# Kernel tuning notes

Hardware: AMD Instinct MI355X
Metric: run time of the kernel (lower is better)

The kernel has to match this reference:

```python
import jax, jax.numpy as jnp
import numpy as np

B, S, D, DV = 64, 2048, 128, 256

def setup_inputs() -> dict:
    key = jax.random.key(0)
    ks = jax.random.split(key, 8)
    queries = jax.random.normal(ks[0], (B, S, D), dtype=jnp.float32)
    keys = jax.random.normal(ks[1], (B, S, D), dtype=jnp.float32)
    values = jax.random.normal(ks[2], (B, S, DV), dtype=jnp.float32)
    valid_lens = jax.random.randint(ks[3], (B,), 1, S + 1)
    # parameters (torch Linear stores weight as [out, in]; we keep math y = x @ W.T)
    w_v = jax.random.normal(ks[4], (2 * D,), dtype=jnp.float32) / np.sqrt(2 * D)   # Linear(256,1,bias=False)
    w2 = jax.random.normal(ks[5], (D, D), dtype=jnp.float32) / np.sqrt(D)          # Linear(128,128,bias=False)
    w_v2_w = jax.random.normal(ks[6], (D,), dtype=jnp.float32) / np.sqrt(D)        # Linear(128,1) weight
    w_v2_b = jax.random.normal(ks[7], (1,), dtype=jnp.float32) / np.sqrt(D)        # Linear(128,1) bias
    return {"queries": queries, "keys": keys, "values": values, "valid_lens": valid_lens,
            "w_v": w_v, "w2": w2, "w_v2_w": w_v2_w, "w_v2_b": w_v2_b}

def reference(queries, keys, values, valid_lens, w_v, w2, w_v2_w, w_v2_b):
    # path 1: concat + tanh + linear score -> [B,S]
    feats = jnp.tanh(jnp.concatenate((queries, keys), axis=-1))      # [B,S,256]
    scores1 = jnp.einsum("bsd,d->bs", feats, w_v)                    # squeeze(2)
    # path 2: linear + tanh + linear(+bias) + softmax over last dim of size 1 (=> all ones, kept faithful)
    feats2 = jnp.tanh(jnp.einsum("bsd,ed->bse", queries, w2))        # [B,S,128]
    s2 = jnp.einsum("bsd,d->bs", feats2, w_v2_w)[..., None] + w_v2_b  # [B,S,1]
    scores2 = jax.nn.softmax(s2, axis=-1)[..., 0]                    # [B,S]
    # blend (detached in original) + softmax over S
    blend = 0.5 * jax.lax.stop_gradient(scores1) + 0.5 * jax.lax.stop_gradient(scores2)
    scores = jax.nn.softmax(blend, axis=-1)[:, None, :]              # [B,1,S]
    # masked softmax with per-batch valid lengths
    mask = jnp.arange(S) < valid_lens[:, None]                       # [B,S]
    attn = jax.nn.softmax(jnp.where(mask[:, None, :], scores, -1e6), axis=-1)  # [B,1,S]
    # dropout is identity in eval mode
    return jnp.einsum("bqs,bsv->bqv", attn, values)                  # [B,1,DV]
```

## Files before the change

### kernel.cpp

```cpp
#include <hip/hip_runtime.h>

#define BB 64
#define SS 2048
#define DD 128
#define DDV 256
#define NCH 32
#define RPC 64

__device__ __forceinline__ float fast_tanh(float x) {
    const float t = __expf(2.0f * x);
    return 1.0f - 2.0f / (t + 1.0f);
}

__global__ __launch_bounds__(256) void k_blend(const float* __restrict__ q,
                                               const float* __restrict__ k,
                                               const float* __restrict__ wv,
                                               float* __restrict__ blend) {
    const int wave = threadIdx.x >> 6;
    const int lane = threadIdx.x & 63;
    const float* src = (lane < 32) ? q : k;
    const float4 w4  = *(const float4*)(wv + lane * 4);
    const int row0 = blockIdx.x * 16 + wave * 4;
#pragma unroll
    for (int i = 0; i < 4; ++i) {
        const int row  = row0 + i;
        const float4 x = *(const float4*)(src + (size_t)row * DD + (lane & 31) * 4);
        float acc = fast_tanh(x.x) * w4.x + fast_tanh(x.y) * w4.y
                  + fast_tanh(x.z) * w4.z + fast_tanh(x.w) * w4.w;
#pragma unroll
        for (int o = 32; o; o >>= 1) acc += __shfl_xor(acc, o, 64);
        if (lane == 0) blend[row] = 0.5f * acc + 0.5f;
    }
}

__global__ __launch_bounds__(1024) void k_weights(float* __restrict__ blend,
                                                  const int* __restrict__ valid) {
    __shared__ float r0[16], r1[16], r2[16], r3[16];
    const int b = blockIdx.x;
    const int t = threadIdx.x;
    const int wid = t >> 6, lane = t & 63;
    float* rowp = blend + (size_t)b * SS;

    const float v0 = rowp[t];
    const float v1 = rowp[t + 1024];

    float m = fmaxf(v0, v1);
#pragma unroll
    for (int o = 32; o; o >>= 1) m = fmaxf(m, __shfl_xor(m, o, 64));
    if (lane == 0) r0[wid] = m;
    __syncthreads();
    float m1 = r0[0];
#pragma unroll
    for (int i = 1; i < 16; i++) m1 = fmaxf(m1, r0[i]);

    const float e0 = expf(v0 - m1), e1 = expf(v1 - m1);
    float s = e0 + e1;
#pragma unroll
    for (int o = 32; o; o >>= 1) s += __shfl_xor(s, o, 64);
    if (lane == 0) r1[wid] = s;
    __syncthreads();
    float Z1 = 0.f;
#pragma unroll
    for (int i = 0; i < 16; i++) Z1 += r1[i];
    const float invZ1 = 1.f / Z1;
    const float p0 = e0 * invZ1, p1 = e1 * invZ1;

    const int L = valid[b];

    float mm = -1e30f;
    if (t < L)        mm = p0;
    if (t + 1024 < L) mm = fmaxf(mm, p1);
#pragma unroll
    for (int o = 32; o; o >>= 1) mm = fmaxf(mm, __shfl_xor(mm, o, 64));
    if (lane == 0) r2[wid] = mm;
    __syncthreads();
    float m2 = r2[0];
#pragma unroll
    for (int i = 1; i < 16; i++) m2 = fmaxf(m2, r2[i]);

    const float f0 = (t < L)        ? expf(p0 - m2) : 0.f;
    const float f1 = (t + 1024 < L) ? expf(p1 - m2) : 0.f;
    float s2 = f0 + f1;
#pragma unroll
    for (int o = 32; o; o >>= 1) s2 += __shfl_xor(s2, o, 64);
    if (lane == 0) r3[wid] = s2;
    __syncthreads();
    float Z2 = 0.f;
#pragma unroll
    for (int i = 0; i < 16; i++) Z2 += r3[i];
    const float invZ2 = 1.f / Z2;

    rowp[t]        = f0 * invZ2;
    rowp[t + 1024] = f1 * invZ2;
}

__global__ __launch_bounds__(256) void k_pv(const float* __restrict__ w,
                                            const float* __restrict__ values,
                                            const int* __restrict__ valid,
                                            float* __restrict__ partial) {
    const int c = blockIdx.x, b = blockIdx.y;
    const int t = threadIdx.x;
    const int wid = t >> 6, lane = t & 63;
    const int s0 = c * RPC;
    __shared__ float wsm[RPC];
    __shared__ float4 sacc[256];

    const int L = valid[b];
    float4 acc = {0.f, 0.f, 0.f, 0.f};
    if (s0 < L) {
        if (t < RPC) wsm[t] = w[(size_t)b * SS + s0 + t];
        __syncthreads();
        float wr[16];
        bool any = false;
#pragma unroll
        for (int i = 0; i < 16; i++) { wr[i] = wsm[wid * 16 + i]; any |= (wr[i] != 0.f); }
        if (any) {
            const float* vb = values + ((size_t)b * SS + s0 + wid * 16) * DDV + lane * 4;
#pragma unroll
            for (int i = 0; i < 16; i++) {
                const float4 v4 = *(const float4*)(vb + (size_t)i * DDV);
                acc.x += wr[i] * v4.x;
                acc.y += wr[i] * v4.y;
                acc.z += wr[i] * v4.z;
                acc.w += wr[i] * v4.w;
            }
        }
    }
    sacc[t] = acc;
    __syncthreads();
    if (t < 64) {
        const float4 a0 = sacc[t], a1 = sacc[t + 64], a2 = sacc[t + 128], a3 = sacc[t + 192];
        float4 r;
        r.x = a0.x + a1.x + a2.x + a3.x;
        r.y = a0.y + a1.y + a2.y + a3.y;
        r.z = a0.z + a1.z + a2.z + a3.z;
        r.w = a0.w + a1.w + a2.w + a3.w;
        *(float4*)(partial + ((size_t)(b * NCH + c)) * 256 + t * 4) = r;
    }
}

__global__ __launch_bounds__(256) void k_reduce(const float* __restrict__ partial,
                                                float* __restrict__ out) {
    const int b = blockIdx.x, t = threadIdx.x;
    float acc = 0.f;
#pragma unroll
    for (int c = 0; c < NCH; c++) acc += partial[((size_t)b * NCH + c) * 256 + t];
    out[(size_t)b * 256 + t] = acc;
}

extern "C" void kernel_launch(void* const* d_in, const int* in_sizes, int n_in,
                              void* d_out, int out_size, void* d_ws, size_t ws_size,
                              hipStream_t stream) {
    const float* q    = (const float*)d_in[0];
    const float* k    = (const float*)d_in[1];
    const float* v    = (const float*)d_in[2];
    const int*   vlen = (const int*)d_in[3];
    const float* wv   = (const float*)d_in[4];

    float* blend   = (float*)d_ws;
    float* partial = blend + (size_t)BB * SS;
    float* out     = (float*)d_out;

    k_blend <<<dim3(BB * SS / 16), dim3(256),  0, stream>>>(q, k, wv, blend);
    k_weights<<<dim3(BB),          dim3(1024), 0, stream>>>(blend, vlen);
    k_pv     <<<dim3(NCH, BB),     dim3(256),  0, stream>>>(blend, v, vlen, partial);
    k_reduce <<<dim3(BB),          dim3(256),  0, stream>>>(partial, out);
}
```

Measured before the change: 46.53 us.

## Compute softmax stats only and recompute weights inside PV kernel

The weights kernel now writes only per-batch softmax statistics (max, inverse sum for both softmaxes) instead of rewriting the full weight row, and the PV kernel recomputes each weight from the blend score and the stats. This removes a full write of the weight buffer. The blend kernel also drops the constant 0.5 offset (it cancels in the softmax), folds the 0.5 scale into the weights, handles 8 rows per wave instead of 4, and uses a hardware reciprocal in tanh. The cost is two extra exps per weight in the PV kernel.

New measurement: 45.22 us. 2.8% less time.

```diff
diff --git a/kernel.cpp b/kernel.cpp
--- a/kernel.cpp
+++ b/kernel.cpp
@@ -9,7 +9,7 @@
 
 __device__ __forceinline__ float fast_tanh(float x) {
     const float t = __expf(2.0f * x);
-    return 1.0f - 2.0f / (t + 1.0f);
+    return 1.0f - 2.0f * __builtin_amdgcn_rcpf(t + 1.0f);
 }
 
 __global__ __launch_bounds__(256) void k_blend(const float* __restrict__ q,
@@ -19,27 +19,29 @@
     const int wave = threadIdx.x >> 6;
     const int lane = threadIdx.x & 63;
     const float* src = (lane < 32) ? q : k;
-    const float4 w4  = *(const float4*)(wv + lane * 4);
-    const int row0 = blockIdx.x * 16 + wave * 4;
+    float4 w4 = *(const float4*)(wv + lane * 4);
+    w4.x *= 0.5f; w4.y *= 0.5f; w4.z *= 0.5f; w4.w *= 0.5f;
+    const int row0 = blockIdx.x * 32 + wave * 8;
+    const float* base = src + (size_t)row0 * DD + (lane & 31) * 4;
 #pragma unroll
-    for (int i = 0; i < 4; ++i) {
-        const int row  = row0 + i;
-        const float4 x = *(const float4*)(src + (size_t)row * DD + (lane & 31) * 4);
+    for (int i = 0; i < 8; ++i) {
+        const float4 x = *(const float4*)(base + (size_t)i * DD);
         float acc = fast_tanh(x.x) * w4.x + fast_tanh(x.y) * w4.y
                   + fast_tanh(x.z) * w4.z + fast_tanh(x.w) * w4.w;
 #pragma unroll
         for (int o = 32; o; o >>= 1) acc += __shfl_xor(acc, o, 64);
-        if (lane == 0) blend[row] = 0.5f * acc + 0.5f;
+        if (lane == 0) blend[row0 + i] = acc;
     }
 }
 
-__global__ __launch_bounds__(1024) void k_weights(float* __restrict__ blend,
-                                                  const int* __restrict__ valid) {
+__global__ __launch_bounds__(1024) void k_stats(const float* __restrict__ blend,
+                                                const int* __restrict__ valid,
+                                                float4* __restrict__ stats) {
     __shared__ float r0[16], r1[16], r2[16], r3[16];
     const int b = blockIdx.x;
     const int t = threadIdx.x;
     const int wid = t >> 6, lane = t & 63;
-    float* rowp = blend + (size_t)b * SS;
+    const float* rowp = blend + (size_t)b * SS;
 
     const float v0 = rowp[t];
     const float v1 = rowp[t + 1024];
@@ -63,13 +65,12 @@
 #pragma unroll
     for (int i = 0; i < 16; i++) Z1 += r1[i];
     const float invZ1 = 1.f / Z1;
-    const float p0 = e0 * invZ1, p1 = e1 * invZ1;
 
     const int L = valid[b];
 
     float mm = -1e30f;
-    if (t < L)        mm = p0;
-    if (t + 1024 < L) mm = fmaxf(mm, p1);
+    if (t < L)        mm = e0 * invZ1;
+    if (t + 1024 < L) mm = fmaxf(mm, e1 * invZ1);
 #pragma unroll
     for (int o = 32; o; o >>= 1) mm = fmaxf(mm, __shfl_xor(mm, o, 64));
     if (lane == 0) r2[wid] = mm;
@@ -78,9 +79,9 @@
 #pragma unroll
     for (int i = 1; i < 16; i++) m2 = fmaxf(m2, r2[i]);
 
-    const float f0 = (t < L)        ? expf(p0 - m2) : 0.f;
-    const float f1 = (t + 1024 < L) ? expf(p1 - m2) : 0.f;
-    float s2 = f0 + f1;
+    float s2 = 0.f;
+    if (t < L)        s2  = expf(e0 * invZ1 - m2);
+    if (t + 1024 < L) s2 += expf(e1 * invZ1 - m2);
 #pragma unroll
     for (int o = 32; o; o >>= 1) s2 += __shfl_xor(s2, o, 64);
     if (lane == 0) r3[wid] = s2;
@@ -88,13 +89,11 @@
     float Z2 = 0.f;
 #pragma unroll
     for (int i = 0; i < 16; i++) Z2 += r3[i];
-    const float invZ2 = 1.f / Z2;
-
-    rowp[t]        = f0 * invZ2;
-    rowp[t + 1024] = f1 * invZ2;
+    if (t == 0) stats[b] = make_float4(m1, invZ1, m2, 1.f / Z2);
 }
 
-__global__ __launch_bounds__(256) void k_pv(const float* __restrict__ w,
+__global__ __launch_bounds__(256) void k_pv(const float* __restrict__ blend,
+                                            const float4* __restrict__ stats,
                                             const float* __restrict__ values,
                                             const int* __restrict__ valid,
                                             float* __restrict__ partial) {
@@ -108,7 +107,14 @@
     const int L = valid[b];
     float4 acc = {0.f, 0.f, 0.f, 0.f};
     if (s0 < L) {
-        if (t < RPC) wsm[t] = w[(size_t)b * SS + s0 + t];
+        const float4 st = stats[b];
+        if (t < RPC) {
+            const int s = s0 + t;
+            float w = 0.f;
+            if (s < L)
+                w = expf(expf(blend[(size_t)b * SS + s] - st.x) * st.y - st.z) * st.w;
+            wsm[t] = w;
+        }
         __syncthreads();
         float wr[16];
         bool any = false;
@@ -157,12 +163,13 @@
     const int*   vlen = (const int*)d_in[3];
     const float* wv   = (const float*)d_in[4];
 
-    float* blend   = (float*)d_ws;
-    float* partial = blend + (size_t)BB * SS;
-    float* out     = (float*)d_out;
+    float*  blend   = (float*)d_ws;
+    float4* stats   = (float4*)(blend + (size_t)BB * SS);
+    float*  partial = (float*)(stats + BB);
+    float*  out     = (float*)d_out;
 
-    k_blend <<<dim3(BB * SS / 16), dim3(256),  0, stream>>>(q, k, wv, blend);
-    k_weights<<<dim3(BB),          dim3(1024), 0, stream>>>(blend, vlen);
-    k_pv     <<<dim3(NCH, BB),     dim3(256),  0, stream>>>(blend, v, vlen, partial);
-    k_reduce <<<dim3(BB),          dim3(256),  0, stream>>>(partial, out);
+    k_blend <<<dim3(BB * SS / 32), dim3(256),  0, stream>>>(q, k, wv, blend);
+    k_stats <<<dim3(BB),           dim3(1024), 0, stream>>>(blend, vlen, stats);
+    k_pv    <<<dim3(NCH, BB),      dim3(256),  0, stream>>>(blend, stats, v, vlen, partial);
+    k_reduce<<<dim3(BB),           dim3(256),  0, stream>>>(partial, out);
 }
```

## Fuse masked softmax and value reduction into one per-batch kernel

Applied to the files above, without the earlier changes.

Merges the weights, partial-PV and reduce kernels into a single kernel with one 1024-thread block per batch. It keeps the softmax weights in LDS and streams the value rows directly to the output, removing the partial buffer and two launches. The blend kernel now handles 32 rows per block, folds the 0.5 scale into the weights, drops the constant offset (safe because softmax is shift-invariant), and uses a hardware reciprocal inside tanh. The trade-off is that the value streaming, the dominant memory traffic, now runs on only 64 blocks, which may leave much of the GPU's bandwidth unused.

Result: slower. 51.40 us (+10.5%).

```diff
diff --git a/kernel.cpp b/kernel.cpp
--- a/kernel.cpp
+++ b/kernel.cpp
@@ -4,12 +4,10 @@
 #define SS 2048
 #define DD 128
 #define DDV 256
-#define NCH 32
-#define RPC 64
 
 __device__ __forceinline__ float fast_tanh(float x) {
     const float t = __expf(2.0f * x);
-    return 1.0f - 2.0f / (t + 1.0f);
+    return 1.0f - 2.0f * __builtin_amdgcn_rcpf(t + 1.0f);
 }
 
 __global__ __launch_bounds__(256) void k_blend(const float* __restrict__ q,
@@ -19,27 +17,32 @@
     const int wave = threadIdx.x >> 6;
     const int lane = threadIdx.x & 63;
     const float* src = (lane < 32) ? q : k;
-    const float4 w4  = *(const float4*)(wv + lane * 4);
-    const int row0 = blockIdx.x * 16 + wave * 4;
+    float4 w4 = *(const float4*)(wv + lane * 4);
+    w4.x *= 0.5f; w4.y *= 0.5f; w4.z *= 0.5f; w4.w *= 0.5f;
+    const int row0 = blockIdx.x * 32 + wave * 8;
+    const float* base = src + (size_t)row0 * DD + (lane & 31) * 4;
 #pragma unroll
-    for (int i = 0; i < 4; ++i) {
-        const int row  = row0 + i;
-        const float4 x = *(const float4*)(src + (size_t)row * DD + (lane & 31) * 4);
+    for (int i = 0; i < 8; ++i) {
+        const float4 x = *(const float4*)(base + (size_t)i * DD);
         float acc = fast_tanh(x.x) * w4.x + fast_tanh(x.y) * w4.y
                   + fast_tanh(x.z) * w4.z + fast_tanh(x.w) * w4.w;
 #pragma unroll
         for (int o = 32; o; o >>= 1) acc += __shfl_xor(acc, o, 64);
-        if (lane == 0) blend[row] = 0.5f * acc + 0.5f;
+        if (lane == 0) blend[row0 + i] = acc;
     }
 }
 
-__global__ __launch_bounds__(1024) void k_weights(float* __restrict__ blend,
-                                                  const int* __restrict__ valid) {
-    __shared__ float r0[16], r1[16], r2[16], r3[16];
+__global__ __launch_bounds__(1024) void k_batch(const float* __restrict__ blend,
+                                                const int* __restrict__ valid,
+                                                const float* __restrict__ values,
+                                                float* __restrict__ out) {
+    __shared__ float  wlds[SS];
+    __shared__ float4 sacc[16][64];
+    __shared__ float  r0[16], r1[16], r2[16], r3[16];
     const int b = blockIdx.x;
     const int t = threadIdx.x;
-    const int wid = t >> 6, lane = t & 63;
-    float* rowp = blend + (size_t)b * SS;
+    const int w = t >> 6, lane = t & 63;
+    const float* rowp = blend + (size_t)b * SS;
 
     const float v0 = rowp[t];
     const float v1 = rowp[t + 1024];
@@ -47,21 +50,21 @@
     float m = fmaxf(v0, v1);
 #pragma unroll
     for (int o = 32; o; o >>= 1) m = fmaxf(m, __shfl_xor(m, o, 64));
-    if (lane == 0) r0[wid] = m;
+    if (lane == 0) r0[w] = m;
     __syncthreads();
     float m1 = r0[0];
 #pragma unroll
-    for (int i = 1; i < 16; i++) m1 = fmaxf(m1, r0[i]);
+    for (int i = 1; i < 16; ++i) m1 = fmaxf(m1, r0[i]);
 
     const float e0 = expf(v0 - m1), e1 = expf(v1 - m1);
     float s = e0 + e1;
 #pragma unroll
     for (int o = 32; o; o >>= 1) s += __shfl_xor(s, o, 64);
-    if (lane == 0) r1[wid] = s;
+    if (lane == 0) r1[w] = s;
     __syncthreads();
     float Z1 = 0.f;
 #pragma unroll
-    for (int i = 0; i < 16; i++) Z1 += r1[i];
+    for (int i = 0; i < 16; ++i) Z1 += r1[i];
     const float invZ1 = 1.f / Z1;
     const float p0 = e0 * invZ1, p1 = e1 * invZ1;
 
@@ -72,80 +75,52 @@
     if (t + 1024 < L) mm = fmaxf(mm, p1);
 #pragma unroll
     for (int o = 32; o; o >>= 1) mm = fmaxf(mm, __shfl_xor(mm, o, 64));
-    if (lane == 0) r2[wid] = mm;
+    if (lane == 0) r2[w] = mm;
     __syncthreads();
     float m2 = r2[0];
 #pragma unroll
-    for (int i = 1; i < 16; i++) m2 = fmaxf(m2, r2[i]);
+    for (int i = 1; i < 16; ++i) m2 = fmaxf(m2, r2[i]);
 
     const float f0 = (t < L)        ? expf(p0 - m2) : 0.f;
     const float f1 = (t + 1024 < L) ? expf(p1 - m2) : 0.f;
     float s2 = f0 + f1;
 #pragma unroll
     for (int o = 32; o; o >>= 1) s2 += __shfl_xor(s2, o, 64);
-    if (lane == 0) r3[wid] = s2;
+    if (lane == 0) r3[w] = s2;
     __syncthreads();
     float Z2 = 0.f;
 #pragma unroll
-    for (int i = 0; i < 16; i++) Z2 += r3[i];
+    for (int i = 0; i < 16; ++i) Z2 += r3[i];
     const float invZ2 = 1.f / Z2;
 
-    rowp[t]        = f0 * invZ2;
-    rowp[t + 1024] = f1 * invZ2;
-}
+    wlds[t]        = f0 * invZ2;
+    wlds[t + 1024] = f1 * invZ2;
+    __syncthreads();
 
-__global__ __launch_bounds__(256) void k_pv(const float* __restrict__ w,
-                                            const float* __restrict__ values,
-                                            const int* __restrict__ valid,
-                                            float* __restrict__ partial) {
-    const int c = blockIdx.x, b = blockIdx.y;
-    const int t = threadIdx.x;
-    const int wid = t >> 6, lane = t & 63;
-    const int s0 = c * RPC;
-    __shared__ float wsm[RPC];
-    __shared__ float4 sacc[256];
+    const int niter = (L > w) ? ((L - w + 15) >> 4) : 0;
+    const float* vb = values + ((size_t)b * SS + w) * DDV + lane * 4;
+    float4 acc = {0.f, 0.f, 0.f, 0.f};
+#pragma unroll 8
+    for (int i = 0; i < niter; ++i) {
+        const float wt = wlds[w + 16 * i];
+        const float4 v4 = *(const float4*)(vb + (size_t)i * 16 * DDV);
+        acc.x += wt * v4.x;
+        acc.y += wt * v4.y;
+        acc.z += wt * v4.z;
+        acc.w += wt * v4.w;
+    }
+    sacc[w][lane] = acc;
+    __syncthreads();
 
-    const int L = valid[b];
-    float4 acc = {0.f, 0.f, 0.f, 0.f};
-    if (s0 < L) {
-        if (t < RPC) wsm[t] = w[(size_t)b * SS + s0 + t];
-        __syncthreads();
-        float wr[16];
-        bool any = false;
+    if (t < 64) {
+        float4 r = {0.f, 0.f, 0.f, 0.f};
 #pragma unroll
-        for (int i = 0; i < 16; i++) { wr[i] = wsm[wid * 16 + i]; any |= (wr[i] != 0.f); }
-        if (any) {
-            const float* vb = values + ((size_t)b * SS + s0 + wid * 16) * DDV + lane * 4;
-#pragma unroll
-            for (int i = 0; i < 16; i++) {
-                const float4 v4 = *(const float4*)(vb + (size_t)i * DDV);
-                acc.x += wr[i] * v4.x;
-                acc.y += wr[i] * v4.y;
-                acc.z += wr[i] * v4.z;
-                acc.w += wr[i] * v4.w;
-            }
+        for (int ww = 0; ww < 16; ++ww) {
+            const float4 a = sacc[ww][t];
+            r.x += a.x; r.y += a.y; r.z += a.z; r.w += a.w;
         }
+        *(float4*)(out + (size_t)b * DDV + t * 4) = r;
     }
-    sacc[t] = acc;
-    __syncthreads();
-    if (t < 64) {
-        const float4 a0 = sacc[t], a1 = sacc[t + 64], a2 = sacc[t + 128], a3 = sacc[t + 192];
-        float4 r;
-        r.x = a0.x + a1.x + a2.x + a3.x;
-        r.y = a0.y + a1.y + a2.y + a3.y;
-        r.z = a0.z + a1.z + a2.z + a3.z;
-        r.w = a0.w + a1.w + a2.w + a3.w;
-        *(float4*)(partial + ((size_t)(b * NCH + c)) * 256 + t * 4) = r;
-    }
-}
-
-__global__ __launch_bounds__(256) void k_reduce(const float* __restrict__ partial,
-                                                float* __restrict__ out) {
-    const int b = blockIdx.x, t = threadIdx.x;
-    float acc = 0.f;
-#pragma unroll
-    for (int c = 0; c < NCH; c++) acc += partial[((size_t)b * NCH + c) * 256 + t];
-    out[(size_t)b * 256 + t] = acc;
 }
 
 extern "C" void kernel_launch(void* const* d_in, const int* in_sizes, int n_in,
@@ -157,12 +132,9 @@
     const int*   vlen = (const int*)d_in[3];
     const float* wv   = (const float*)d_in[4];
 
-    float* blend   = (float*)d_ws;
-    float* partial = blend + (size_t)BB * SS;
-    float* out     = (float*)d_out;
+    float* blend = (float*)d_ws;
+    float* out   = (float*)d_out;
 
-    k_blend <<<dim3(BB * SS / 16), dim3(256),  0, stream>>>(q, k, wv, blend);
-    k_weights<<<dim3(BB),          dim3(1024), 0, stream>>>(blend, vlen);
-    k_pv     <<<dim3(NCH, BB),     dim3(256),  0, stream>>>(blend, v, vlen, partial);
-    k_reduce <<<dim3(BB),          dim3(256),  0, stream>>>(partial, out);
+    k_blend<<<dim3(BB * SS / 32), dim3(256),  0, stream>>>(q, k, wv, blend);
+    k_batch<<<dim3(BB),           dim3(1024), 0, stream>>>(blend, vlen, v, out);
 }
```
